# Kernel tuning notes

Hardware: AMD Instinct MI355X
Metric: run time of the kernel (lower is better)

Reference implementation:

```python
import jax, jax.numpy as jnp
import numpy as np

SCALE_FACTORS = (1, 2, 4)
N, T, F = 4096, 128, 128
MARKET = 64
MIX = sum(T // k for k in SCALE_FACTORS)  # 224


def hardswish(x):
    return x * jnp.clip(x + 3.0, 0.0, 6.0) * (1.0 / 6.0)


def layernorm2d(x, g, b, eps=1e-5):
    # LayerNorm with normalized_shape == last two dims (as in torch nn.LayerNorm((A, B)))
    mu = jnp.mean(x, axis=(-2, -1), keepdims=True)
    var = jnp.var(x, axis=(-2, -1), keepdims=True)
    return (x - mu) * jax.lax.rsqrt(var + eps) * g + b


def setup_inputs() -> dict:
    key = jax.random.key(0)
    ks = jax.random.split(key, 32)
    inp = {"x": jax.random.normal(ks[0], (N, T, F), jnp.float32)}
    i = 1
    for si, k in enumerate(SCALE_FACTORS):
        tk = T // k
        inp[f"cw{si}"] = jax.random.normal(ks[i], (F, F, k), jnp.float32) * 0.05; i += 1
        inp[f"cb{si}"] = jnp.zeros((F,), jnp.float32)
        inp[f"lg{si}"] = jnp.ones((tk, F), jnp.float32)
        inp[f"lb{si}"] = jnp.zeros((tk, F), jnp.float32)
        inp[f"L1_{si}"] = jax.random.normal(ks[i], (tk, tk), jnp.float32) * 0.01; i += 1
        inp[f"L2_{si}"] = jax.random.normal(ks[i], (tk, tk), jnp.float32) * 0.01; i += 1
    inp["fc_w"] = jax.random.normal(ks[i], (1, F), jnp.float32) * 0.05; i += 1
    inp["fc_b"] = jnp.zeros((1,), jnp.float32)
    inp["sm_lg"] = jnp.ones((N, MIX), jnp.float32)
    inp["sm_lb"] = jnp.zeros((N, MIX), jnp.float32)
    inp["M1"] = jax.random.normal(ks[i], (MARKET, N), jnp.float32); i += 1
    inp["M2"] = jax.random.normal(ks[i], (N, MARKET), jnp.float32); i += 1
    inp["sm_fc_w"] = jax.random.normal(ks[i], (1, 2 * MIX), jnp.float32) * 0.02; i += 1
    inp["sm_fc_b"] = jnp.zeros((1,), jnp.float32)
    return inp


def _forward(x, cw0, cb0, lg0, lb0, L1_0, L2_0,
             cw1, cb1, lg1, lb1, L1_1, L2_1,
             cw2, cb2, lg2, lb2, L1_2, L2_2,
             fc_w, fc_b, sm_lg, sm_lb, M1, M2, sm_fc_w, sm_fc_b):
    n, t, f = x.shape
    per_scale = ((cw0, cb0, lg0, lb0, L1_0, L2_0),
                 (cw1, cb1, lg1, lb1, L1_1, L2_1),
                 (cw2, cb2, lg2, lb2, L1_2, L2_2))
    parts = []
    for k, (cw, cb, lg, lb, L1, L2) in zip(SCALE_FACTORS, per_scale):
        tk = t // k
        # Conv1d(kernel=k, stride=k) == blockwise contraction over non-overlapping windows
        xr = x.transpose(0, 2, 1).reshape(n, f, tk, k)          # (n, F_in, tk, k)
        xt = jnp.einsum('nitk,oik->nto', xr, cw) + cb            # (n, tk, F)
        # TimeMixing: ragged prefix loop == single lower-triangular matmul over time
        mask = jnp.tril(jnp.ones((tk, tk), x.dtype))
        h = layernorm2d(xt, lg, lb)
        u = hardswish(jnp.einsum('ts,nsf->ntf', L1 * mask, h))
        v = jnp.einsum('ts,nsf->ntf', L2 * mask, u)
        xt = xt + v
        parts.append(xt @ fc_w[0] + fc_b[0])                     # (n, tk)
    h = jnp.concatenate(parts, axis=1)                           # (n, MIX)
    # StockMixing
    hn = layernorm2d(h, sm_lg, sm_lb)
    z = M2 @ hardswish(M1 @ hn)                                  # (n, MIX)
    out = jnp.concatenate([h, h + z], axis=1)                    # (n, 2*MIX)
    return out @ sm_fc_w[0][:, None] + sm_fc_b                   # (n, 1)


def reference(x, cw0, cb0, lg0, lb0, L1_0, L2_0,
              cw1, cb1, lg1, lb1, L1_1, L2_1,
              cw2, cb2, lg2, lb2, L1_2, L2_2,
              fc_w, fc_b, sm_lg, sm_lb, M1, M2, sm_fc_w, sm_fc_b):
    return _forward(x, cw0, cb0, lg0, lb0, L1_0, L2_0,
                    cw1, cb1, lg1, lb1, L1_1, L2_1,
                    cw2, cb2, lg2, lb2, L1_2, L2_2,
                    fc_w, fc_b, sm_lg, sm_lb, M1, M2, sm_fc_w, sm_fc_b)
```

## Files before the change

kernel.cpp:

```cpp
#include <hip/hip_runtime.h>
#include <stdint.h>

typedef __attribute__((ext_vector_type(8))) short short8;
typedef __attribute__((ext_vector_type(4))) float f32x4;
typedef __attribute__((ext_vector_type(4))) unsigned short us4;

__device__ __forceinline__ unsigned short f2bf(float f) {
  union { float f; unsigned int i; } v; v.f = f;
  return (unsigned short)((v.i + 0x7FFFu + ((v.i >> 16) & 1u)) >> 16);
}
__device__ __forceinline__ float hswish(float x) {
  float t = fminf(fmaxf(x + 3.f, 0.f), 6.f);
  return x * t * (1.f / 6.f);
}
__device__ __forceinline__ short8 ldcvt8(const float* __restrict__ p) {
  float4 v0 = *(const float4*)p;
  float4 v1 = *(const float4*)(p + 4);
  short8 r;
  r[0] = (short)f2bf(v0.x); r[1] = (short)f2bf(v0.y);
  r[2] = (short)f2bf(v0.z); r[3] = (short)f2bf(v0.w);
  r[4] = (short)f2bf(v1.x); r[5] = (short)f2bf(v1.y);
  r[6] = (short)f2bf(v1.z); r[7] = (short)f2bf(v1.w);
  return r;
}

__global__ void prep_kernel(const float* __restrict__ cw0, const float* __restrict__ cw1,
                            const float* __restrict__ cw2,
                            const float* __restrict__ L1_0, const float* __restrict__ L2_0,
                            const float* __restrict__ L1_1, const float* __restrict__ L2_1,
                            const float* __restrict__ L1_2, const float* __restrict__ L2_2,
                            unsigned short* __restrict__ ws16) {
  int idx = blockIdx.x * 256 + threadIdx.x;
  if (idx < 16384) {
    ws16[idx] = f2bf(cw0[idx]);
  } else if (idx < 49152) {
    int t = idx - 16384; int o = t >> 8, m = t & 255, j = m >> 7, i = m & 127;
    ws16[idx] = f2bf(cw1[(o * 128 + i) * 2 + j]);
  } else if (idx < 114688) {
    int t = idx - 49152; int o = t >> 9, m = t & 511, j = m >> 7, i = m & 127;
    ws16[idx] = f2bf(cw2[(o * 128 + i) * 4 + j]);
  } else if (idx < 212992) {
    int u = idx - 114688; int which = u >> 14; int e = u & 16383;
    int t = e >> 7, s = e & 127;
    float val = 0.f;
    if (which == 0)      { if (s <= t) val = L1_0[t * 128 + s]; }
    else if (which == 1) { if (s <= t) val = L2_0[t * 128 + s]; }
    else if (which == 2) { if ((s >> 6) == (t >> 6) && (s & 63) <= (t & 63)) val = L1_1[(t & 63) * 64 + (s & 63)]; }
    else if (which == 3) { if ((s >> 6) == (t >> 6) && (s & 63) <= (t & 63)) val = L2_1[(t & 63) * 64 + (s & 63)]; }
    else if (which == 4) { if ((s >> 5) == (t >> 5) && (s & 31) <= (t & 31)) val = L1_2[(t & 31) * 32 + (s & 31)]; }
    else                 { if ((s >> 5) == (t >> 5) && (s & 31) <= (t & 31)) val = L2_2[(t & 31) * 32 + (s & 31)]; }
    ws16[idx] = f2bf(val);
  }
}

__global__ void xcvt_kernel(const float* __restrict__ x, unsigned short* __restrict__ xbf) {
  const float4* x4 = (const float4*)x;
  us4* o4 = (us4*)xbf;
#pragma unroll
  for (int j = 0; j < 4; ++j) {
    int idx = blockIdx.x * 1024 + j * 256 + threadIdx.x;
    float4 v = x4[idx];
    us4 p; p[0] = f2bf(v.x); p[1] = f2bf(v.y); p[2] = f2bf(v.z); p[3] = f2bf(v.w);
    o4[idx] = p;
  }
}

template <bool XBF>
__device__ __forceinline__ short8 load_a(const float* __restrict__ xf,
                                         const unsigned short* __restrict__ xb, int off) {
  if constexpr (XBF) return *(const short8*)&xb[off];
  else return ldcvt8(xf + off);
}

template <int S, bool XBF>
__launch_bounds__(256, 3)
__global__ void s1_tile(const float* __restrict__ xf, const unsigned short* __restrict__ xb,
                        const float* __restrict__ cb, const float* __restrict__ lg,
                        const float* __restrict__ lb,
                        const float* __restrict__ fc_w, const float* __restrict__ fc_b,
                        const unsigned short* __restrict__ cwLT,
                        const unsigned short* __restrict__ L1blk,
                        const unsigned short* __restrict__ L2blk,
                        float* __restrict__ h_out) {
  constexpr int K = 128 << S;
  constexpr int LOG2TK = 7 - S;
  constexpr int TKM = (128 >> S) - 1;
  constexpr int SAMPLES = 1 << S;
  constexpr int OFF = (S == 0) ? 0 : (S == 1 ? 128 : 192);
  constexpr int NK = K / 32;
  constexpr int GSH = 3 - S;
  constexpr float INVD = 1.f / (float)((TKM + 1) * 128);

  __shared__ unsigned short HT[128 * 128];
  __shared__ float scr[272];
  float* part = scr + 128;

  const int tid = threadIdx.x, wave = tid >> 6, lane = tid & 63;
  const int quad = lane >> 4, l16 = lane & 15;
  const int Tb = (wave & 1) * 4, Ob = (wave >> 1) * 4;
  const int n0 = blockIdx.x << S;
  const int abase = n0 * 16384;
  const float fcb = fc_b[0];

  if (tid < 128) { scr[tid] = fc_w[tid]; part[tid] = 0.f; }
  else if (tid < 144) scr[tid + 128] = 0.f;
  __syncthreads();

  f32x4 acc[4][4];
#pragma unroll
  for (int tt = 0; tt < 4; ++tt)
#pragma unroll
    for (int oo = 0; oo < 4; ++oo) acc[tt][oo] = (f32x4){0.f, 0.f, 0.f, 0.f};
#pragma unroll
  for (int ks = 0; ks < NK; ++ks) {
    short8 a[4];
#pragma unroll
    for (int tt = 0; tt < 4; ++tt)
      a[tt] = load_a<XBF>(xf, xb, abase + ((Tb + tt) * 16 + l16) * K + ks * 32 + quad * 8);
#pragma unroll
    for (int oo = 0; oo < 4; ++oo) {
      short8 b = *(const short8*)&cwLT[((Ob + oo) * 16 + l16) * K + ks * 32 + quad * 8];
#pragma unroll
      for (int tt = 0; tt < 4; ++tt)
        acc[tt][oo] = __builtin_amdgcn_mfma_f32_16x16x32_bf16(a[tt], b, acc[tt][oo], 0, 0, 0);
    }
  }

  float ts[4] = {0.f, 0.f, 0.f, 0.f}, tq[4] = {0.f, 0.f, 0.f, 0.f};
#pragma unroll
  for (int oo = 0; oo < 4; ++oo) {
    float cbv = cb[(Ob + oo) * 16 + l16];
#pragma unroll
    for (int tt = 0; tt < 4; ++tt)
#pragma unroll
      for (int r = 0; r < 4; ++r) {
        float v = acc[tt][oo][r] + cbv;
        acc[tt][oo][r] = v;
        ts[tt] += v; tq[tt] += v * v;
      }
  }
  {
    constexpr int GPW = (S == 2) ? 2 : 1;
    float gs[2] = {0.f, 0.f}, gq[2] = {0.f, 0.f};
#pragma unroll
    for (int tt = 0; tt < 4; ++tt) {
      int gl = (S == 2) ? (tt >> 1) : 0;
      gs[gl] += ts[tt]; gq[gl] += tq[tt];
    }
#pragma unroll
    for (int j = 0; j < GPW; ++j) {
      float s = gs[j], q = gq[j];
#pragma unroll
      for (int m = 32; m >= 1; m >>= 1) { s += __shfl_xor(s, m); q += __shfl_xor(q, m); }
      if (lane == 0) {
        int g = (Tb >> GSH) + j;
        atomicAdd(&scr[256 + 2 * g], s);
        atomicAdd(&scr[257 + 2 * g], q);
      }
    }
  }
  __syncthreads();
  if (tid < SAMPLES) {
    float mu = scr[256 + 2 * tid] * INVD;
    float var = scr[257 + 2 * tid] * INVD - mu * mu;
    scr[264 + tid] = mu; scr[268 + tid] = rsqrtf(var + 1e-5f);
  }
  __syncthreads();

#pragma unroll
  for (int tt = 0; tt < 4; ++tt)
#pragma unroll
    for (int r = 0; r < 4; ++r) {
      float v = 0.f;
#pragma unroll
      for (int oo = 0; oo < 4; ++oo) v += acc[tt][oo][r] * scr[(Ob + oo) * 16 + l16];
      v += __shfl_xor(v, 1); v += __shfl_xor(v, 2);
      v += __shfl_xor(v, 4); v += __shfl_xor(v, 8);
      if (l16 == 0) atomicAdd(&part[(Tb + tt) * 16 + quad * 4 + r], v);
    }

#pragma unroll
  for (int tt = 0; tt < 4; ++tt) {
    int tile = Tb + tt, g = tile >> GSH;
    float mu = scr[264 + g], rs = scr[268 + g];
    int tlb = (tile * 16) & TKM;
#pragma unroll
    for (int oo = 0; oo < 4; ++oo) {
      int f = (Ob + oo) * 16 + l16;
      int kf = (f ^ (f >> 3)) & 15;
#pragma unroll
      for (int r = 0; r < 4; ++r) {
        int t = tile * 16 + quad * 4 + r;
        int tl = tlb + quad * 4 + r;
        float hv = (acc[tt][oo][r] - mu) * rs * lg[tl * 128 + f] + lb[tl * 128 + f];
        HT[f * 128 + ((((t >> 3) ^ kf) << 3) | (t & 7))] = f2bf(hv);
      }
    }
  }
  __syncthreads();

  f32x4 u[4][4];
#pragma unroll
  for (int tt = 0; tt < 4; ++tt)
#pragma unroll
    for (int oo = 0; oo < 4; ++oo) u[tt][oo] = (f32x4){0.f, 0.f, 0.f, 0.f};
#pragma unroll
  for (int ks = 0; ks < 4; ++ks) {
    short8 a[4]; bool act[4]; bool any = false;
#pragma unroll
    for (int tt = 0; tt < 4; ++tt) {
      int tile = Tb + tt, g = tile >> GSH;
      act[tt] = (ks * 32 <= tile * 16 + 15) && (ks * 32 + 31 >= (g << LOG2TK));
      if (act[tt]) { a[tt] = *(const short8*)&L1blk[(tile * 16 + l16) * 128 + ks * 32 + quad * 8]; any = true; }
    }
    if (!any) continue;
#pragma unroll
    for (int oo = 0; oo < 4; ++oo) {
      int f = (Ob + oo) * 16 + l16;
      int kf = (f ^ (f >> 3)) & 15;
      short8 b = *(const short8*)&HT[f * 128 + (((ks * 4 + quad) ^ kf) << 3)];
#pragma unroll
      for (int tt = 0; tt < 4; ++tt)
        if (act[tt]) u[tt][oo] = __builtin_amdgcn_mfma_f32_16x16x32_bf16(a[tt], b, u[tt][oo], 0, 0, 0);
    }
  }
  __syncthreads();

#pragma unroll
  for (int tt = 0; tt < 4; ++tt) {
    int tile = Tb + tt;
#pragma unroll
    for (int oo = 0; oo < 4; ++oo) {
      int f = (Ob + oo) * 16 + l16;
      int kf = (f ^ (f >> 3)) & 15;
#pragma unroll
      for (int r = 0; r < 4; ++r) {
        int t = tile * 16 + quad * 4 + r;
        HT[f * 128 + ((((t >> 3) ^ kf) << 3) | (t & 7))] = f2bf(hswish(u[tt][oo][r]));
      }
    }
  }
  __syncthreads();

#pragma unroll
  for (int tt = 0; tt < 4; ++tt)
#pragma unroll
    for (int oo = 0; oo < 4; ++oo) u[tt][oo] = (f32x4){0.f, 0.f, 0.f, 0.f};
#pragma unroll
  for (int ks = 0; ks < 4; ++ks) {
    short8 a[4]; bool act[4]; bool any = false;
#pragma unroll
    for (int tt = 0; tt < 4; ++tt) {
      int tile = Tb + tt, g = tile >> GSH;
      act[tt] = (ks * 32 <= tile * 16 + 15) && (ks * 32 + 31 >= (g << LOG2TK));
      if (act[tt]) { a[tt] = *(const short8*)&L2blk[(tile * 16 + l16) * 128 + ks * 32 + quad * 8]; any = true; }
    }
    if (!any) continue;
#pragma unroll
    for (int oo = 0; oo < 4; ++oo) {
      int f = (Ob + oo) * 16 + l16;
      int kf = (f ^ (f >> 3)) & 15;
      short8 b = *(const short8*)&HT[f * 128 + (((ks * 4 + quad) ^ kf) << 3)];
#pragma unroll
      for (int tt = 0; tt < 4; ++tt)
        if (act[tt]) u[tt][oo] = __builtin_amdgcn_mfma_f32_16x16x32_bf16(a[tt], b, u[tt][oo], 0, 0, 0);
    }
  }

#pragma unroll
  for (int tt = 0; tt < 4; ++tt)
#pragma unroll
    for (int r = 0; r < 4; ++r) {
      float v = 0.f;
#pragma unroll
      for (int oo = 0; oo < 4; ++oo) v += u[tt][oo][r] * scr[(Ob + oo) * 16 + l16];
      v += __shfl_xor(v, 1); v += __shfl_xor(v, 2);
      v += __shfl_xor(v, 4); v += __shfl_xor(v, 8);
      if (l16 == 0) atomicAdd(&part[(Tb + tt) * 16 + quad * 4 + r], v);
    }
  __syncthreads();

  if (tid < 128) {
    int g = tid >> LOG2TK, tl = tid & TKM;
    h_out[(size_t)(n0 + g) * 224 + OFF + tl] = part[tid] + fcb;
  }
}

__global__ void stats_kernel(const float* __restrict__ h, float* __restrict__ stats) {
  int base = blockIdx.x * 4096;
  float s = 0.f, ss = 0.f;
  for (int j = 0; j < 16; ++j) {
    float v = h[base + j * 256 + threadIdx.x];
    s += v; ss += v * v;
  }
  int lane = threadIdx.x & 63, wave = threadIdx.x >> 6;
#pragma unroll
  for (int m = 32; m >= 1; m >>= 1) { s += __shfl_xor(s, m); ss += __shfl_xor(ss, m); }
  __shared__ float red[8];
  if (lane == 0) { red[wave * 2] = s; red[wave * 2 + 1] = ss; }
  __syncthreads();
  if (threadIdx.x == 0) {
    atomicAdd(&stats[0], red[0] + red[2] + red[4] + red[6]);
    atomicAdd(&stats[1], red[1] + red[3] + red[5] + red[7]);
  }
}

__global__ void mix1_kernel(const float* __restrict__ h,
                            const float* __restrict__ sm_lg,
                            const float* __restrict__ sm_lb,
                            const float* __restrict__ M1,
                            const float* __restrict__ stats,
                            float* __restrict__ A) {
  const int m = blockIdx.x, seg = blockIdx.y;
  const int r = threadIdx.x & 63, ch = threadIdx.x >> 6;
  const float inv = 1.f / 917504.f;
  float mu = stats[0] * inv;
  float var = stats[1] * inv - mu * mu;
  float rsig = rsqrtf(var + 1e-5f);
  float acc = 0.f;
  int n0 = seg * 1024 + ch * 256;
  for (int i = 0; i < 256; ++i) {
    int n = n0 + i;
    float hn = (h[n * 224 + m] - mu) * rsig * sm_lg[n * 224 + m] + sm_lb[n * 224 + m];
    acc += M1[r * 4096 + n] * hn;
  }
  __shared__ float red[256];
  red[threadIdx.x] = acc;
  __syncthreads();
  if (threadIdx.x < 64)
    atomicAdd(&A[threadIdx.x * 224 + m],
              red[threadIdx.x] + red[64 + threadIdx.x] + red[128 + threadIdx.x] + red[192 + threadIdx.x]);
}

__global__ void mix2_kernel(const float* __restrict__ A,
                            const float* __restrict__ sm_fc_w,
                            float* __restrict__ cvec) {
  int r = threadIdx.x & 63, ch = threadIdx.x >> 6;
  float acc = 0.f;
  for (int j = ch; j < 224; j += 4)
    acc += hswish(A[r * 224 + j]) * sm_fc_w[224 + j];
  __shared__ float red[256];
  red[threadIdx.x] = acc;
  __syncthreads();
  if (threadIdx.x < 64)
    cvec[threadIdx.x] = red[threadIdx.x] + red[64 + threadIdx.x] + red[128 + threadIdx.x] + red[192 + threadIdx.x];
}

__global__ void out_kernel(const float* __restrict__ h,
                           const float* __restrict__ M2,
                           const float* __restrict__ cvec,
                           const float* __restrict__ sm_fc_w,
                           const float* __restrict__ sm_fc_b,
                           float* __restrict__ out) {
  int wave = threadIdx.x >> 6, lane = threadIdx.x & 63;
  int n = blockIdx.x * 4 + wave;
  float acc = M2[n * 64 + lane] * cvec[lane];
  for (int j = lane; j < 224; j += 64)
    acc += h[n * 224 + j] * (sm_fc_w[j] + sm_fc_w[224 + j]);
#pragma unroll
  for (int m = 32; m >= 1; m >>= 1) acc += __shfl_xor(acc, m);
  if (lane == 0) out[n] = acc + sm_fc_b[0];
}

extern "C" void kernel_launch(void* const* d_in, const int* in_sizes, int n_in,
                              void* d_out, int out_size, void* d_ws, size_t ws_size,
                              hipStream_t stream) {
  const float* x      = (const float*)d_in[0];
  const float* cw0    = (const float*)d_in[1];
  const float* cb0    = (const float*)d_in[2];
  const float* lg0    = (const float*)d_in[3];
  const float* lb0    = (const float*)d_in[4];
  const float* L1_0   = (const float*)d_in[5];
  const float* L2_0   = (const float*)d_in[6];
  const float* cw1    = (const float*)d_in[7];
  const float* cb1    = (const float*)d_in[8];
  const float* lg1    = (const float*)d_in[9];
  const float* lb1    = (const float*)d_in[10];
  const float* L1_1   = (const float*)d_in[11];
  const float* L2_1   = (const float*)d_in[12];
  const float* cw2    = (const float*)d_in[13];
  const float* cb2    = (const float*)d_in[14];
  const float* lg2    = (const float*)d_in[15];
  const float* lb2    = (const float*)d_in[16];
  const float* L1_2   = (const float*)d_in[17];
  const float* L2_2   = (const float*)d_in[18];
  const float* fc_w   = (const float*)d_in[19];
  const float* fc_b   = (const float*)d_in[20];
  const float* sm_lg  = (const float*)d_in[21];
  const float* sm_lb  = (const float*)d_in[22];
  const float* M1     = (const float*)d_in[23];
  const float* M2     = (const float*)d_in[24];
  const float* sm_fc_w = (const float*)d_in[25];
  const float* sm_fc_b = (const float*)d_in[26];

  char* ws = (char*)d_ws;
  unsigned short* ws16 = (unsigned short*)ws;
  float* h     = (float*)(ws + 425984);
  float* stats = (float*)(ws + 4096000);
  float* A     = (float*)(ws + 4096256);
  float* cvec  = (float*)(ws + 4153600);
  unsigned short* xbf = (unsigned short*)(ws + 4194304);
  const bool use_xbf = ws_size >= 138412032ULL;

  const unsigned short* cwLT0 = ws16;
  const unsigned short* cwLT1 = ws16 + 16384;
  const unsigned short* cwLT2 = ws16 + 49152;
  const unsigned short* L1b0 = ws16 + 114688;
  const unsigned short* L2b0 = ws16 + 131072;
  const unsigned short* L1b1 = ws16 + 147456;
  const unsigned short* L2b1 = ws16 + 163840;
  const unsigned short* L1b2 = ws16 + 180224;
  const unsigned short* L2b2 = ws16 + 196608;

  prep_kernel<<<832, 256, 0, stream>>>(cw0, cw1, cw2, L1_0, L2_0, L1_1, L2_1, L1_2, L2_2, ws16);

  if (use_xbf) {
    xcvt_kernel<<<16384, 256, 0, stream>>>(x, xbf);
    s1_tile<0, true><<<4096, 256, 0, stream>>>(x, xbf, cb0, lg0, lb0, fc_w, fc_b, cwLT0, L1b0, L2b0, h);
    s1_tile<1, true><<<2048, 256, 0, stream>>>(x, xbf, cb1, lg1, lb1, fc_w, fc_b, cwLT1, L1b1, L2b1, h);
    s1_tile<2, true><<<1024, 256, 0, stream>>>(x, xbf, cb2, lg2, lb2, fc_w, fc_b, cwLT2, L1b2, L2b2, h);
  } else {
    s1_tile<0, false><<<4096, 256, 0, stream>>>(x, xbf, cb0, lg0, lb0, fc_w, fc_b, cwLT0, L1b0, L2b0, h);
    s1_tile<1, false><<<2048, 256, 0, stream>>>(x, xbf, cb1, lg1, lb1, fc_w, fc_b, cwLT1, L1b1, L2b1, h);
    s1_tile<2, false><<<1024, 256, 0, stream>>>(x, xbf, cb2, lg2, lb2, fc_w, fc_b, cwLT2, L1b2, L2b2, h);
  }

  hipMemsetAsync(ws + 4096000, 0, 57600, stream);
  stats_kernel<<<224, 256, 0, stream>>>(h, stats);
  mix1_kernel<<<dim3(224, 4), 256, 0, stream>>>(h, sm_lg, sm_lb, M1, stats, A);
  mix2_kernel<<<1, 256, 0, stream>>>(A, sm_fc_w, cvec);
  out_kernel<<<1024, 256, 0, stream>>>(h, M2, cvec, sm_fc_w, sm_fc_b, (float*)d_out);
}
```

Measured before the change: 902.0 us.

## Repartition s1 waves by feature, fuse output stats, transpose M1 and LN params

Each wave now owns all 128 time rows for 32 output features. The LDS buffer HT is then written and read only by the same wave, so the barriers between the conv, L1 and L2 stages are removed. Global stats for the stock-mixing layernorm are accumulated inside the s1 kernels into 32 slots, which drops stats_kernel and the large memset. M1 and the per-scale layernorm gain and bias are pre-transposed in prep for coalesced loads, and mix1 writes A directly instead of using atomics. The trade-off is that each wave loads the full x tile, doubling A-operand load traffic per block.

```diff
diff --git a/kernel.cpp b/kernel.cpp
--- a/kernel.cpp
+++ b/kernel.cpp
@@ -4,6 +4,7 @@
 typedef __attribute__((ext_vector_type(8))) short short8;
 typedef __attribute__((ext_vector_type(4))) float f32x4;
 typedef __attribute__((ext_vector_type(4))) unsigned short us4;
+typedef unsigned short ushort_t;
 
 __device__ __forceinline__ unsigned short f2bf(float f) {
   union { float f; unsigned int i; } v; v.f = f;
@@ -24,12 +25,36 @@
   return r;
 }
 
+#define WS16_OFF      0ULL
+#define M1T_OFF       425984ULL
+#define LGT0_OFF      1474560ULL
+#define LBT0_OFF      1540096ULL
+#define LGT1_OFF      1605632ULL
+#define LBT1_OFF      1638400ULL
+#define LGT2_OFF      1671168ULL
+#define LBT2_OFF      1687552ULL
+#define H_OFF         1703936ULL
+#define STATS_OFF     5373952ULL
+#define A_OFF         5374208ULL
+#define CVEC_OFF      5431552ULL
+#define XBF_OFF       8388608ULL
+#define WS_NEED       142606336ULL
+
 __global__ void prep_kernel(const float* __restrict__ cw0, const float* __restrict__ cw1,
                             const float* __restrict__ cw2,
                             const float* __restrict__ L1_0, const float* __restrict__ L2_0,
                             const float* __restrict__ L1_1, const float* __restrict__ L2_1,
                             const float* __restrict__ L1_2, const float* __restrict__ L2_2,
-                            unsigned short* __restrict__ ws16) {
+                            const float* __restrict__ M1,
+                            const float* __restrict__ lg0, const float* __restrict__ lb0,
+                            const float* __restrict__ lg1, const float* __restrict__ lb1,
+                            const float* __restrict__ lg2, const float* __restrict__ lb2,
+                            char* __restrict__ ws) {
+  unsigned short* ws16 = (unsigned short*)(ws + WS16_OFF);
+  float* m1t  = (float*)(ws + M1T_OFF);
+  float* lgT0 = (float*)(ws + LGT0_OFF); float* lbT0 = (float*)(ws + LBT0_OFF);
+  float* lgT1 = (float*)(ws + LGT1_OFF); float* lbT1 = (float*)(ws + LBT1_OFF);
+  float* lgT2 = (float*)(ws + LGT2_OFF); float* lbT2 = (float*)(ws + LBT2_OFF);
   int idx = blockIdx.x * 256 + threadIdx.x;
   if (idx < 16384) {
     ws16[idx] = f2bf(cw0[idx]);
@@ -50,6 +75,21 @@
     else if (which == 4) { if ((s >> 5) == (t >> 5) && (s & 31) <= (t & 31)) val = L1_2[(t & 31) * 32 + (s & 31)]; }
     else                 { if ((s >> 5) == (t >> 5) && (s & 31) <= (t & 31)) val = L2_2[(t & 31) * 32 + (s & 31)]; }
     ws16[idx] = f2bf(val);
+  } else if (idx < 475136) {
+    int e = idx - 212992; int n = e >> 6, r = e & 63;
+    m1t[e] = M1[r * 4096 + n];
+  } else if (idx < 491520) {
+    int e = idx - 475136; int f = e >> 7, t = e & 127; lgT0[e] = lg0[t * 128 + f];
+  } else if (idx < 507904) {
+    int e = idx - 491520; int f = e >> 7, t = e & 127; lbT0[e] = lb0[t * 128 + f];
+  } else if (idx < 516096) {
+    int e = idx - 507904; int f = e >> 6, t = e & 63;  lgT1[e] = lg1[t * 128 + f];
+  } else if (idx < 524288) {
+    int e = idx - 516096; int f = e >> 6, t = e & 63;  lbT1[e] = lb1[t * 128 + f];
+  } else if (idx < 528384) {
+    int e = idx - 524288; int f = e >> 5, t = e & 31;  lgT2[e] = lg2[t * 128 + f];
+  } else if (idx < 532480) {
+    int e = idx - 528384; int f = e >> 5, t = e & 31;  lbT2[e] = lb2[t * 128 + f];
   }
 }
 
@@ -65,271 +105,259 @@
   }
 }
 
-template <bool XBF>
-__device__ __forceinline__ short8 load_a(const float* __restrict__ xf,
-                                         const unsigned short* __restrict__ xb, int off) {
-  if constexpr (XBF) return *(const short8*)&xb[off];
-  else return ldcvt8(xf + off);
-}
-
 template <int S, bool XBF>
 __launch_bounds__(256, 3)
-__global__ void s1_tile(const float* __restrict__ xf, const unsigned short* __restrict__ xb,
-                        const float* __restrict__ cb, const float* __restrict__ lg,
-                        const float* __restrict__ lb,
-                        const float* __restrict__ fc_w, const float* __restrict__ fc_b,
-                        const unsigned short* __restrict__ cwLT,
-                        const unsigned short* __restrict__ L1blk,
-                        const unsigned short* __restrict__ L2blk,
-                        float* __restrict__ h_out) {
+__global__ void s1_wp(const float* __restrict__ xf, const unsigned short* __restrict__ xb,
+                      const float* __restrict__ cb,
+                      const float* __restrict__ lgT, const float* __restrict__ lbT,
+                      const float* __restrict__ fc_w, const float* __restrict__ fc_b,
+                      const unsigned short* __restrict__ cwLT,
+                      const unsigned short* __restrict__ L1blk,
+                      const unsigned short* __restrict__ L2blk,
+                      float* __restrict__ h_out, float* __restrict__ stats) {
   constexpr int K = 128 << S;
-  constexpr int LOG2TK = 7 - S;
-  constexpr int TKM = (128 >> S) - 1;
+  constexpr int TK = 128 >> S;
+  constexpr int L2TK = 7 - S;
+  constexpr int GSH = 3 - S;
   constexpr int SAMPLES = 1 << S;
   constexpr int OFF = (S == 0) ? 0 : (S == 1 ? 128 : 192);
   constexpr int NK = K / 32;
-  constexpr int GSH = 3 - S;
-  constexpr float INVD = 1.f / (float)((TKM + 1) * 128);
+  constexpr float INVD = 1.f / (float)(TK * 128);
 
   __shared__ unsigned short HT[128 * 128];
-  __shared__ float scr[272];
+  __shared__ float scr[288];
   float* part = scr + 128;
 
   const int tid = threadIdx.x, wave = tid >> 6, lane = tid & 63;
   const int quad = lane >> 4, l16 = lane & 15;
-  const int Tb = (wave & 1) * 4, Ob = (wave >> 1) * 4;
   const int n0 = blockIdx.x << S;
-  const int abase = n0 * 16384;
-  const float fcb = fc_b[0];
+  const size_t xbase = (size_t)n0 * 16384;
+  const int fo0 = (wave * 2) * 16 + l16;
+  const int fo1 = (wave * 2 + 1) * 16 + l16;
+  const int kf0 = (fo0 ^ (fo0 >> 3)) & 15;
+  const int kf1 = (fo1 ^ (fo1 >> 3)) & 15;
 
   if (tid < 128) { scr[tid] = fc_w[tid]; part[tid] = 0.f; }
-  else if (tid < 144) scr[tid + 128] = 0.f;
-  __syncthreads();
-
-  f32x4 acc[4][4];
-#pragma unroll
-  for (int tt = 0; tt < 4; ++tt)
-#pragma unroll
-    for (int oo = 0; oo < 4; ++oo) acc[tt][oo] = (f32x4){0.f, 0.f, 0.f, 0.f};
+
+  f32x4 acc[8][2];
+#pragma unroll
+  for (int tt = 0; tt < 8; ++tt) {
+    acc[tt][0] = (f32x4){0.f, 0.f, 0.f, 0.f};
+    acc[tt][1] = (f32x4){0.f, 0.f, 0.f, 0.f};
+  }
 #pragma unroll
   for (int ks = 0; ks < NK; ++ks) {
-    short8 a[4];
-#pragma unroll
-    for (int tt = 0; tt < 4; ++tt)
-      a[tt] = load_a<XBF>(xf, xb, abase + ((Tb + tt) * 16 + l16) * K + ks * 32 + quad * 8);
-#pragma unroll
-    for (int oo = 0; oo < 4; ++oo) {
-      short8 b = *(const short8*)&cwLT[((Ob + oo) * 16 + l16) * K + ks * 32 + quad * 8];
-#pragma unroll
-      for (int tt = 0; tt < 4; ++tt)
-        acc[tt][oo] = __builtin_amdgcn_mfma_f32_16x16x32_bf16(a[tt], b, acc[tt][oo], 0, 0, 0);
-    }
-  }
-
-  float ts[4] = {0.f, 0.f, 0.f, 0.f}, tq[4] = {0.f, 0.f, 0.f, 0.f};
-#pragma unroll
-  for (int oo = 0; oo < 4; ++oo) {
-    float cbv = cb[(Ob + oo) * 16 + l16];
-#pragma unroll
-    for (int tt = 0; tt < 4; ++tt)
+    short8 b0 = *(const short8*)&cwLT[fo0 * K + ks * 32 + quad * 8];
+    short8 b1 = *(const short8*)&cwLT[fo1 * K + ks * 32 + quad * 8];
+    short8 a[8];
+#pragma unroll
+    for (int tt = 0; tt < 8; ++tt) {
+      size_t off = xbase + (size_t)(tt * 16 + l16) * K + ks * 32 + quad * 8;
+      if constexpr (XBF) a[tt] = *(const short8*)&xb[off];
+      else a[tt] = ldcvt8(xf + off);
+    }
+#pragma unroll
+    for (int tt = 0; tt < 8; ++tt) {
+      acc[tt][0] = __builtin_amdgcn_mfma_f32_16x16x32_bf16(a[tt], b0, acc[tt][0], 0, 0, 0);
+      acc[tt][1] = __builtin_amdgcn_mfma_f32_16x16x32_bf16(a[tt], b1, acc[tt][1], 0, 0, 0);
+    }
+  }
+
+  const float cbv0 = cb[fo0], cbv1 = cb[fo1];
+  {
+    float gs[SAMPLES], gq[SAMPLES];
+#pragma unroll
+    for (int g = 0; g < SAMPLES; ++g) { gs[g] = 0.f; gq[g] = 0.f; }
+#pragma unroll
+    for (int tt = 0; tt < 8; ++tt) {
+      int g = tt >> GSH;
 #pragma unroll
       for (int r = 0; r < 4; ++r) {
-        float v = acc[tt][oo][r] + cbv;
-        acc[tt][oo][r] = v;
-        ts[tt] += v; tq[tt] += v * v;
-      }
-  }
-  {
-    constexpr int GPW = (S == 2) ? 2 : 1;
-    float gs[2] = {0.f, 0.f}, gq[2] = {0.f, 0.f};
-#pragma unroll
-    for (int tt = 0; tt < 4; ++tt) {
-      int gl = (S == 2) ? (tt >> 1) : 0;
-      gs[gl] += ts[tt]; gq[gl] += tq[tt];
-    }
-#pragma unroll
-    for (int j = 0; j < GPW; ++j) {
-      float s = gs[j], q = gq[j];
+        float v0 = acc[tt][0][r] + cbv0;
+        float v1 = acc[tt][1][r] + cbv1;
+        acc[tt][0][r] = v0; acc[tt][1][r] = v1;
+        gs[g] += v0 + v1; gq[g] += v0 * v0 + v1 * v1;
+      }
+    }
+#pragma unroll
+    for (int g = 0; g < SAMPLES; ++g) {
+      float s = gs[g], q = gq[g];
 #pragma unroll
       for (int m = 32; m >= 1; m >>= 1) { s += __shfl_xor(s, m); q += __shfl_xor(q, m); }
       if (lane == 0) {
-        int g = (Tb >> GSH) + j;
-        atomicAdd(&scr[256 + 2 * g], s);
-        atomicAdd(&scr[257 + 2 * g], q);
+        scr[256 + (wave * SAMPLES + g) * 2] = s;
+        scr[257 + (wave * SAMPLES + g) * 2] = q;
       }
     }
   }
   __syncthreads();
-  if (tid < SAMPLES) {
-    float mu = scr[256 + 2 * tid] * INVD;
-    float var = scr[257 + 2 * tid] * INVD - mu * mu;
-    scr[264 + tid] = mu; scr[268 + tid] = rsqrtf(var + 1e-5f);
-  }
-  __syncthreads();
-
-#pragma unroll
-  for (int tt = 0; tt < 4; ++tt)
+
+  float mu[SAMPLES], rs[SAMPLES];
+#pragma unroll
+  for (int g = 0; g < SAMPLES; ++g) {
+    float s = 0.f, q = 0.f;
+#pragma unroll
+    for (int w = 0; w < 4; ++w) {
+      s += scr[256 + (w * SAMPLES + g) * 2];
+      q += scr[257 + (w * SAMPLES + g) * 2];
+    }
+    float m = s * INVD;
+    mu[g] = m; rs[g] = rsqrtf(q * INVD - m * m + 1e-5f);
+  }
+
+#pragma unroll
+  for (int tt = 0; tt < 8; ++tt)
 #pragma unroll
     for (int r = 0; r < 4; ++r) {
-      float v = 0.f;
-#pragma unroll
-      for (int oo = 0; oo < 4; ++oo) v += acc[tt][oo][r] * scr[(Ob + oo) * 16 + l16];
+      float v = acc[tt][0][r] * scr[fo0] + acc[tt][1][r] * scr[fo1];
       v += __shfl_xor(v, 1); v += __shfl_xor(v, 2);
       v += __shfl_xor(v, 4); v += __shfl_xor(v, 8);
-      if (l16 == 0) atomicAdd(&part[(Tb + tt) * 16 + quad * 4 + r], v);
-    }
-
-#pragma unroll
-  for (int tt = 0; tt < 4; ++tt) {
-    int tile = Tb + tt, g = tile >> GSH;
-    float mu = scr[264 + g], rs = scr[268 + g];
-    int tlb = (tile * 16) & TKM;
-#pragma unroll
-    for (int oo = 0; oo < 4; ++oo) {
-      int f = (Ob + oo) * 16 + l16;
-      int kf = (f ^ (f >> 3)) & 15;
+      if (l16 == 0) atomicAdd(&part[tt * 16 + quad * 4 + r], v);
+    }
+
+#pragma unroll
+  for (int tt = 0; tt < 8; ++tt) {
+    int g = tt >> GSH;
+    int tb = tt * 16 + quad * 4;
+    int tlb = tb & (TK - 1);
+#pragma unroll
+    for (int oo = 0; oo < 2; ++oo) {
+      int f = oo ? fo1 : fo0;
+      int kf = oo ? kf1 : kf0;
+      float4 lg4 = *(const float4*)&lgT[f * TK + tlb];
+      float4 lb4 = *(const float4*)&lbT[f * TK + tlb];
 #pragma unroll
       for (int r = 0; r < 4; ++r) {
-        int t = tile * 16 + quad * 4 + r;
-        int tl = tlb + quad * 4 + r;
-        float hv = (acc[tt][oo][r] - mu) * rs * lg[tl * 128 + f] + lb[tl * 128 + f];
+        int t = tb + r;
+        float hv = (acc[tt][oo][r] - mu[g]) * rs[g] * (&lg4.x)[r] + (&lb4.x)[r];
         HT[f * 128 + ((((t >> 3) ^ kf) << 3) | (t & 7))] = f2bf(hv);
       }
     }
   }
-  __syncthreads();
-
-  f32x4 u[4][4];
-#pragma unroll
-  for (int tt = 0; tt < 4; ++tt)
-#pragma unroll
-    for (int oo = 0; oo < 4; ++oo) u[tt][oo] = (f32x4){0.f, 0.f, 0.f, 0.f};
+
+  f32x4 u[8][2];
+#pragma unroll
+  for (int tt = 0; tt < 8; ++tt) {
+    u[tt][0] = (f32x4){0.f, 0.f, 0.f, 0.f};
+    u[tt][1] = (f32x4){0.f, 0.f, 0.f, 0.f};
+  }
 #pragma unroll
   for (int ks = 0; ks < 4; ++ks) {
-    short8 a[4]; bool act[4]; bool any = false;
-#pragma unroll
-    for (int tt = 0; tt < 4; ++tt) {
-      int tile = Tb + tt, g = tile >> GSH;
-      act[tt] = (ks * 32 <= tile * 16 + 15) && (ks * 32 + 31 >= (g << LOG2TK));
-      if (act[tt]) { a[tt] = *(const short8*)&L1blk[(tile * 16 + l16) * 128 + ks * 32 + quad * 8]; any = true; }
-    }
-    if (!any) continue;
-#pragma unroll
-    for (int oo = 0; oo < 4; ++oo) {
-      int f = (Ob + oo) * 16 + l16;
-      int kf = (f ^ (f >> 3)) & 15;
-      short8 b = *(const short8*)&HT[f * 128 + (((ks * 4 + quad) ^ kf) << 3)];
-#pragma unroll
-      for (int tt = 0; tt < 4; ++tt)
-        if (act[tt]) u[tt][oo] = __builtin_amdgcn_mfma_f32_16x16x32_bf16(a[tt], b, u[tt][oo], 0, 0, 0);
-    }
-  }
-  __syncthreads();
-
-#pragma unroll
-  for (int tt = 0; tt < 4; ++tt) {
-    int tile = Tb + tt;
-#pragma unroll
-    for (int oo = 0; oo < 4; ++oo) {
-      int f = (Ob + oo) * 16 + l16;
-      int kf = (f ^ (f >> 3)) & 15;
+    short8 a[8];
+#pragma unroll
+    for (int tt = 0; tt < 8; ++tt) {
+      constexpr int dummy = 0; (void)dummy;
+      int g = tt >> GSH;
+      bool act = (ks * 32 <= tt * 16 + 15) && (ks * 32 + 32 > (g << L2TK));
+      if (act) a[tt] = *(const short8*)&L1blk[(tt * 16 + l16) * 128 + ks * 32 + quad * 8];
+    }
+    short8 b0 = *(const short8*)&HT[fo0 * 128 + (((ks * 4 + quad) ^ kf0) << 3)];
+    short8 b1 = *(const short8*)&HT[fo1 * 128 + (((ks * 4 + quad) ^ kf1) << 3)];
+#pragma unroll
+    for (int tt = 0; tt < 8; ++tt) {
+      int g = tt >> GSH;
+      bool act = (ks * 32 <= tt * 16 + 15) && (ks * 32 + 32 > (g << L2TK));
+      if (act) {
+        u[tt][0] = __builtin_amdgcn_mfma_f32_16x16x32_bf16(a[tt], b0, u[tt][0], 0, 0, 0);
+        u[tt][1] = __builtin_amdgcn_mfma_f32_16x16x32_bf16(a[tt], b1, u[tt][1], 0, 0, 0);
+      }
+    }
+  }
+
+#pragma unroll
+  for (int tt = 0; tt < 8; ++tt) {
+    int tb = tt * 16 + quad * 4;
+#pragma unroll
+    for (int oo = 0; oo < 2; ++oo) {
+      int f = oo ? fo1 : fo0;
+      int kf = oo ? kf1 : kf0;
 #pragma unroll
       for (int r = 0; r < 4; ++r) {
-        int t = tile * 16 + quad * 4 + r;
+        int t = tb + r;
         HT[f * 128 + ((((t >> 3) ^ kf) << 3) | (t & 7))] = f2bf(hswish(u[tt][oo][r]));
       }
     }
   }
-  __syncthreads();
-
-#pragma unroll
-  for (int tt = 0; tt < 4; ++tt)
-#pragma unroll
-    for (int oo = 0; oo < 4; ++oo) u[tt][oo] = (f32x4){0.f, 0.f, 0.f, 0.f};
+
+#pragma unroll
+  for (int tt = 0; tt < 8; ++tt) {
+    u[tt][0] = (f32x4){0.f, 0.f, 0.f, 0.f};
+    u[tt][1] = (f32x4){0.f, 0.f, 0.f, 0.f};
+  }
 #pragma unroll
   for (int ks = 0; ks < 4; ++ks) {
-    short8 a[4]; bool act[4]; bool any = false;
-#pragma unroll
-    for (int tt = 0; tt < 4; ++tt) {
-      int tile = Tb + tt, g = tile >> GSH;
-      act[tt] = (ks * 32 <= tile * 16 + 15) && (ks * 32 + 31 >= (g << LOG2TK));
-      if (act[tt]) { a[tt] = *(const short8*)&L2blk[(tile * 16 + l16) * 128 + ks * 32 + quad * 8]; any = true; }
-    }
-    if (!any) continue;
-#pragma unroll
-    for (int oo = 0; oo < 4; ++oo) {
-      int f = (Ob + oo) * 16 + l16;
-      int kf = (f ^ (f >> 3)) & 15;
-      short8 b = *(const short8*)&HT[f * 128 + (((ks * 4 + quad) ^ kf) << 3)];
-#pragma unroll
-      for (int tt = 0; tt < 4; ++tt)
-        if (act[tt]) u[tt][oo] = __builtin_amdgcn_mfma_f32_16x16x32_bf16(a[tt], b, u[tt][oo], 0, 0, 0);
-    }
-  }
-
-#pragma unroll
-  for (int tt = 0; tt < 4; ++tt)
+    short8 a[8];
+#pragma unroll
+    for (int tt = 0; tt < 8; ++tt) {
+      int g = tt >> GSH;
+      bool act = (ks * 32 <= tt * 16 + 15) && (ks * 32 + 32 > (g << L2TK));
+      if (act) a[tt] = *(const short8*)&L2blk[(tt * 16 + l16) * 128 + ks * 32 + quad * 8];
+    }
+    short8 b0 = *(const short8*)&HT[fo0 * 128 + (((ks * 4 + quad) ^ kf0) << 3)];
+    short8 b1 = *(const short8*)&HT[fo1 * 128 + (((ks * 4 + quad) ^ kf1) << 3)];
+#pragma unroll
+    for (int tt = 0; tt < 8; ++tt) {
+      int g = tt >> GSH;
+      bool act = (ks * 32 <= tt * 16 + 15) && (ks * 32 + 32 > (g << L2TK));
+      if (act) {
+        u[tt][0] = __builtin_amdgcn_mfma_f32_16x16x32_bf16(a[tt], b0, u[tt][0], 0, 0, 0);
+        u[tt][1] = __builtin_amdgcn_mfma_f32_16x16x32_bf16(a[tt], b1, u[tt][1], 0, 0, 0);
+      }
+    }
+  }
+
+#pragma unroll
+  for (int tt = 0; tt < 8; ++tt)
 #pragma unroll
     for (int r = 0; r < 4; ++r) {
-      float v = 0.f;
-#pragma unroll
-      for (int oo = 0; oo < 4; ++oo) v += u[tt][oo][r] * scr[(Ob + oo) * 16 + l16];
+      float v = u[tt][0][r] * scr[fo0] + u[tt][1][r] * scr[fo1];
       v += __shfl_xor(v, 1); v += __shfl_xor(v, 2);
       v += __shfl_xor(v, 4); v += __shfl_xor(v, 8);
-      if (l16 == 0) atomicAdd(&part[(Tb + tt) * 16 + quad * 4 + r], v);
+      if (l16 == 0) atomicAdd(&part[tt * 16 + quad * 4 + r], v);
     }
   __syncthreads();
 
   if (tid < 128) {
-    int g = tid >> LOG2TK, tl = tid & TKM;
-    h_out[(size_t)(n0 + g) * 224 + OFF + tl] = part[tid] + fcb;
-  }
-}
-
-__global__ void stats_kernel(const float* __restrict__ h, float* __restrict__ stats) {
-  int base = blockIdx.x * 4096;
-  float s = 0.f, ss = 0.f;
-  for (int j = 0; j < 16; ++j) {
-    float v = h[base + j * 256 + threadIdx.x];
-    s += v; ss += v * v;
-  }
-  int lane = threadIdx.x & 63, wave = threadIdx.x >> 6;
-#pragma unroll
-  for (int m = 32; m >= 1; m >>= 1) { s += __shfl_xor(s, m); ss += __shfl_xor(ss, m); }
-  __shared__ float red[8];
-  if (lane == 0) { red[wave * 2] = s; red[wave * 2 + 1] = ss; }
-  __syncthreads();
-  if (threadIdx.x == 0) {
-    atomicAdd(&stats[0], red[0] + red[2] + red[4] + red[6]);
-    atomicAdd(&stats[1], red[1] + red[3] + red[5] + red[7]);
+    float val = part[tid] + fc_b[0];
+    int g = tid >> L2TK, tl = tid & (TK - 1);
+    h_out[(size_t)(n0 + g) * 224 + OFF + tl] = val;
+    float s = val, q = val * val;
+#pragma unroll
+    for (int m = 32; m >= 1; m >>= 1) { s += __shfl_xor(s, m); q += __shfl_xor(q, m); }
+    if (lane == 0) {
+      int slot = blockIdx.x & 31;
+      atomicAdd(&stats[2 * slot], s);
+      atomicAdd(&stats[2 * slot + 1], q);
+    }
   }
 }
 
 __global__ void mix1_kernel(const float* __restrict__ h,
                             const float* __restrict__ sm_lg,
                             const float* __restrict__ sm_lb,
-                            const float* __restrict__ M1,
+                            const float* __restrict__ m1t,
                             const float* __restrict__ stats,
                             float* __restrict__ A) {
-  const int m = blockIdx.x, seg = blockIdx.y;
-  const int r = threadIdx.x & 63, ch = threadIdx.x >> 6;
+  const int m = blockIdx.x;
+  const int r = threadIdx.x & 63, c = threadIdx.x >> 6;
+  float S = 0.f, Q = 0.f;
+#pragma unroll
+  for (int s = 0; s < 32; ++s) { S += stats[2 * s]; Q += stats[2 * s + 1]; }
   const float inv = 1.f / 917504.f;
-  float mu = stats[0] * inv;
-  float var = stats[1] * inv - mu * mu;
-  float rsig = rsqrtf(var + 1e-5f);
+  float mu = S * inv;
+  float rsig = rsqrtf(Q * inv - mu * mu + 1e-5f);
   float acc = 0.f;
-  int n0 = seg * 1024 + ch * 256;
-  for (int i = 0; i < 256; ++i) {
-    int n = n0 + i;
+  for (int i = 0; i < 1024; ++i) {
+    int n = c * 1024 + i;
     float hn = (h[n * 224 + m] - mu) * rsig * sm_lg[n * 224 + m] + sm_lb[n * 224 + m];
-    acc += M1[r * 4096 + n] * hn;
+    acc += m1t[n * 64 + r] * hn;
   }
   __shared__ float red[256];
   red[threadIdx.x] = acc;
   __syncthreads();
   if (threadIdx.x < 64)
-    atomicAdd(&A[threadIdx.x * 224 + m],
-              red[threadIdx.x] + red[64 + threadIdx.x] + red[128 + threadIdx.x] + red[192 + threadIdx.x]);
+    A[threadIdx.x * 224 + m] =
+        red[threadIdx.x] + red[64 + threadIdx.x] + red[128 + threadIdx.x] + red[192 + threadIdx.x];
 }
 
 __global__ void mix2_kernel(const float* __restrict__ A,
@@ -394,13 +422,17 @@
   const float* sm_fc_b = (const float*)d_in[26];
 
   char* ws = (char*)d_ws;
-  unsigned short* ws16 = (unsigned short*)ws;
-  float* h     = (float*)(ws + 425984);
-  float* stats = (float*)(ws + 4096000);
-  float* A     = (float*)(ws + 4096256);
-  float* cvec  = (float*)(ws + 4153600);
-  unsigned short* xbf = (unsigned short*)(ws + 4194304);
-  const bool use_xbf = ws_size >= 138412032ULL;
+  unsigned short* ws16 = (unsigned short*)(ws + WS16_OFF);
+  float* m1t   = (float*)(ws + M1T_OFF);
+  float* lgT0  = (float*)(ws + LGT0_OFF); float* lbT0 = (float*)(ws + LBT0_OFF);
+  float* lgT1  = (float*)(ws + LGT1_OFF); float* lbT1 = (float*)(ws + LBT1_OFF);
+  float* lgT2  = (float*)(ws + LGT2_OFF); float* lbT2 = (float*)(ws + LBT2_OFF);
+  float* h     = (float*)(ws + H_OFF);
+  float* stats = (float*)(ws + STATS_OFF);
+  float* A     = (float*)(ws + A_OFF);
+  float* cvec  = (float*)(ws + CVEC_OFF);
+  unsigned short* xbf = (unsigned short*)(ws + XBF_OFF);
+  const bool use_xbf = ws_size >= WS_NEED;
 
   const unsigned short* cwLT0 = ws16;
   const unsigned short* cwLT1 = ws16 + 16384;
@@ -412,22 +444,22 @@
   const unsigned short* L1b2 = ws16 + 180224;
   const unsigned short* L2b2 = ws16 + 196608;
 
-  prep_kernel<<<832, 256, 0, stream>>>(cw0, cw1, cw2, L1_0, L2_0, L1_1, L2_1, L1_2, L2_2, ws16);
+  prep_kernel<<<2080, 256, 0, stream>>>(cw0, cw1, cw2, L1_0, L2_0, L1_1, L2_1, L1_2, L2_2,
+                                        M1, lg0, lb0, lg1, lb1, lg2, lb2, ws);
+  hipMemsetAsync(stats, 0, 256, stream);
 
   if (use_xbf) {
     xcvt_kernel<<<16384, 256, 0, stream>>>(x, xbf);
-    s1_tile<0, true><<<4096, 256, 0, stream>>>(x, xbf, cb0, lg0, lb0, fc_w, fc_b, cwLT0, L1b0, L2b0, h);
-    s1_tile<1, true><<<2048, 256, 0, stream>>>(x, xbf, cb1, lg1, lb1, fc_w, fc_b, cwLT1, L1b1, L2b1, h);
-    s1_tile<2, true><<<1024, 256, 0, stream>>>(x, xbf, cb2, lg2, lb2, fc_w, fc_b, cwLT2, L1b2, L2b2, h);
+    s1_wp<0, true><<<4096, 256, 0, stream>>>(x, xbf, cb0, lgT0, lbT0, fc_w, fc_b, cwLT0, L1b0, L2b0, h, stats);
+    s1_wp<1, true><<<2048, 256, 0, stream>>>(x, xbf, cb1, lgT1, lbT1, fc_w, fc_b, cwLT1, L1b1, L2b1, h, stats);
+    s1_wp<2, true><<<1024, 256, 0, stream>>>(x, xbf, cb2, lgT2, lbT2, fc_w, fc_b, cwLT2, L1b2, L2b2, h, stats);
   } else {
-    s1_tile<0, false><<<4096, 256, 0, stream>>>(x, xbf, cb0, lg0, lb0, fc_w, fc_b, cwLT0, L1b0, L2b0, h);
-    s1_tile<1, false><<<2048, 256, 0, stream>>>(x, xbf, cb1, lg1, lb1, fc_w, fc_b, cwLT1, L1b1, L2b1, h);
-    s1_tile<2, false><<<1024, 256, 0, stream>>>(x, xbf, cb2, lg2, lb2, fc_w, fc_b, cwLT2, L1b2, L2b2, h);
-  }
-
-  hipMemsetAsync(ws + 4096000, 0, 57600, stream);
-  stats_kernel<<<224, 256, 0, stream>>>(h, stats);
-  mix1_kernel<<<dim3(224, 4), 256, 0, stream>>>(h, sm_lg, sm_lb, M1, stats, A);
+    s1_wp<0, false><<<4096, 256, 0, stream>>>(x, xbf, cb0, lgT0, lbT0, fc_w, fc_b, cwLT0, L1b0, L2b0, h, stats);
+    s1_wp<1, false><<<2048, 256, 0, stream>>>(x, xbf, cb1, lgT1, lbT1, fc_w, fc_b, cwLT1, L1b1, L2b1, h, stats);
+    s1_wp<2, false><<<1024, 256, 0, stream>>>(x, xbf, cb2, lgT2, lbT2, fc_w, fc_b, cwLT2, L1b2, L2b2, h, stats);
+  }
+
+  mix1_kernel<<<224, 256, 0, stream>>>(h, sm_lg, sm_lb, m1t, stats, A);
   mix2_kernel<<<1, 256, 0, stream>>>(A, sm_fc_w, cvec);
   out_kernel<<<1024, 256, 0, stream>>>(h, M2, cvec, sm_fc_w, sm_fc_b, (float*)d_out);
 }
```

Result: slower. 1.198 ms (+32.8%).
